# Kernel tuning notes

Hardware: AMD Instinct MI355X
Metric: run time of the kernel (lower is better)

The kernel has to match this reference:

```python
import jax, jax.numpy as jnp
import numpy as np

N_NODES = 100000
N_EDGES = 3200000
IN_FEATS = 128
HIDDEN = 64
N_CLASSES = 16


def gcn_conv(x, src, dst, W, b, num_nodes):
    """PyG GCNConv (default settings): add self-loops, symmetric norm,
    linear transform, scatter-sum aggregation at dst, then bias."""
    # degree counts include self-loops (fill value 1.0)
    deg = jnp.zeros((num_nodes,), x.dtype).at[dst].add(1.0) + 1.0
    dinv = jax.lax.rsqrt(deg)  # deg >= 1, no inf handling needed
    h = x @ W  # [N, out]
    # edge messages: norm(src,dst) * h[src], aggregated at dst
    norm = dinv[src] * dinv[dst]  # [E]
    msg = h[src] * norm[:, None]  # [E, out]
    out = jax.ops.segment_sum(msg, dst, num_segments=num_nodes)
    # self-loop contribution: norm = dinv[i]^2
    out = out + h * (dinv * dinv)[:, None]
    return out + b


def setup_inputs() -> dict:
    key = jax.random.key(0)
    k1, k2, k3, k4 = jax.random.split(key, 4)
    x = jax.random.normal(k1, (N_NODES, IN_FEATS), dtype=jnp.float32)
    edge_index = jax.random.randint(k2, (2, N_EDGES), 0, N_NODES, dtype=jnp.int64)
    W1 = jax.random.normal(k3, (IN_FEATS, HIDDEN), dtype=jnp.float32) * (1.0 / np.sqrt(IN_FEATS))
    b1 = jnp.zeros((HIDDEN,), jnp.float32)
    W2 = jax.random.normal(k4, (HIDDEN, N_CLASSES), dtype=jnp.float32) * (1.0 / np.sqrt(HIDDEN))
    b2 = jnp.zeros((N_CLASSES,), jnp.float32)
    return {"x": x, "edge_index": edge_index, "W1": W1, "b1": b1, "W2": W2, "b2": b2}


def reference(x, edge_index, W1, b1, W2, b2):
    src, dst = edge_index[0], edge_index[1]
    h = gcn_conv(x, src, dst, W1, b1, N_NODES)
    h = jax.nn.relu(h)  # dropout is identity in eval mode
    out = gcn_conv(h, src, dst, W2, b2, N_NODES)
    return out
```

## Files before the change

kernel.cpp:

```cpp
#include <hip/hip_runtime.h>
#include <hip/hip_fp16.h>
#include <stdint.h>

#define N_NODES   100000
#define N_HALF    50000
#define N_EDGES   3200000
#define F_IN      128
#define F_HID     64
#define F_OUT     16

typedef _Float16 h2v __attribute__((ext_vector_type(2)));
typedef _Float16 h4v __attribute__((ext_vector_type(4)));

#define BSHIFT    8
#define NBUCK     391
#define NBLK_P    640
#define CHUNK_E   (N_EDGES / NBLK_P)
#define PSTRIDE   9856

#define G1_TM     128
#define G1_BLOCKS ((N_NODES + G1_TM - 1) / G1_TM)
#define XS_LD     132

#define OFF_RS       0
#define OFF_LEN      400000
#define OFF_DINV     800000
#define OFF_GCNT     1200000
#define OFF_CSR      1201616
#define OFF_HS1      8909008
#define OFF_OUT1A    21709008
#define OFF_OUT1B    34509008
#define OFF_HS2      47309008
#define OFF_PAIRS    OFF_OUT1A

__device__ __forceinline__ int edge_src(const void* ei, int is64, int e) {
    return is64 ? (int)((const long long*)ei)[e] : ((const int*)ei)[e];
}
__device__ __forceinline__ int edge_dst(const void* ei, int is64, int e) {
    return is64 ? (int)((const long long*)ei)[N_EDGES + e]
                : ((const int*)ei)[N_EDGES + e];
}

__global__ __launch_bounds__(256) void k_partition(const void* __restrict__ ei,
                                                   int* __restrict__ gcnt,
                                                   unsigned* __restrict__ pairs) {
    __shared__ unsigned long long st[CHUNK_E];
    __shared__ int h[NBUCK];
    __shared__ int cur[NBUCK];
    __shared__ int is64s;
    int t = threadIdx.x;
    if (t == 0) {
        const unsigned* u = (const unsigned*)ei;
        int ok = 1;
        for (int i = 0; i < 64; ++i) {
            unsigned lo = u[2 * i], hi = u[2 * i + 1];
            if (hi != 0u || lo >= 100000u) { ok = 0; break; }
        }
        is64s = ok;
    }
    for (int i = t; i < NBUCK; i += 256) h[i] = 0;
    __syncthreads();
    int is64 = is64s;
    int base = blockIdx.x * CHUNK_E;
    for (int i = t; i < CHUNK_E; i += 256) {
        int s = edge_src(ei, is64, base + i);
        int d = edge_dst(ei, is64, base + i);
        st[i] = ((unsigned long long)(unsigned)s << 32) | (unsigned)d;
        atomicAdd(&h[d >> BSHIFT], 1);
    }
    __syncthreads();
    for (int i = t; i < NBUCK; i += 256) {
        int c = h[i];
        cur[i] = c ? atomicAdd(&gcnt[i], c) : 0;
    }
    __syncthreads();
    for (int i = t; i < CHUNK_E; i += 256) {
        unsigned long long v = st[i];
        unsigned s = (unsigned)(v >> 32);
        unsigned d = (unsigned)v;
        int b = d >> BSHIFT;
        int p = atomicAdd(&cur[b], 1);
        if (p < PSTRIDE)
            pairs[b * PSTRIDE + p] = (s << 8) | (d & 255u);
    }
}

__global__ __launch_bounds__(512) void k_build(const unsigned* __restrict__ pairs,
                                               const int* __restrict__ gcnt,
                                               int* __restrict__ rowstart,
                                               int* __restrict__ lens,
                                               float* __restrict__ dinv,
                                               unsigned short* __restrict__ csr) {
    __shared__ int c0S[256], c1S[256], scanS[256], pos0[256], pos1[256];
    int b = blockIdx.x, t = threadIdx.x;
    if (t < 256) { c0S[t] = 0; c1S[t] = 0; }
    __syncthreads();
    int tot = gcnt[b]; if (tot > PSTRIDE) tot = PSTRIDE;
    int base = b * PSTRIDE;
    for (int i = t; i < tot; i += 512) {
        unsigned pr = pairs[base + i];
        if ((pr >> 8) < (unsigned)N_HALF) atomicAdd(&c0S[pr & 255u], 1);
        else                              atomicAdd(&c1S[pr & 255u], 1);
    }
    __syncthreads();
    int tpad = 0, p0a = 0;
    if (t < 256) {
        p0a = (c0S[t] + 3) & ~3;
        tpad = p0a + ((c1S[t] + 3) & ~3);
        scanS[t] = tpad;
    }
    __syncthreads();
    for (int off = 1; off < 256; off <<= 1) {
        int add = 0;
        if (t < 256 && t >= off) add = scanS[t - off];
        __syncthreads();
        if (t < 256) scanS[t] += add;
        __syncthreads();
    }
    if (t < 256) {
        int rs = base + scanS[t] - tpad;
        pos0[t] = rs;
        pos1[t] = rs + p0a;
        int d = (b << BSHIFT) + t;
        if (d < N_NODES) {
            rowstart[d] = rs;
            lens[d] = c0S[t] | (c1S[t] << 16);
            dinv[d] = rsqrtf((float)(c0S[t] + c1S[t]) + 1.0f);
        }
    }
    __syncthreads();
    for (int i = t; i < tot; i += 512) {
        unsigned pr = pairs[base + i];
        unsigned s = pr >> 8;
        int d = pr & 255u;
        if (s < (unsigned)N_HALF) {
            int p = atomicAdd(&pos0[d], 1);
            csr[p] = (unsigned short)s;
        } else {
            int p = atomicAdd(&pos1[d], 1);
            csr[p] = (unsigned short)(s - N_HALF);
        }
    }
}

__global__ __launch_bounds__(256) void k_gemm1(const float* __restrict__ x,
                                               const float* __restrict__ W1,
                                               const float* __restrict__ dinv,
                                               __half* __restrict__ hs1) {
    __shared__ float xsT[64 * XS_LD];
    __shared__ float ws[64 * 64];
    int t = threadIdx.x;
    int nblock = blockIdx.x * G1_TM;
    int ng = t >> 4, og = t & 15;
    int n0 = ng * 8;
    float acc[8][4] = {};

    int snode = nblock + (t >> 1);
    int koff = (t & 1) * 32;
    int nl = t >> 1;

    for (int chunk = 0; chunk < 2; ++chunk) {
        int kbase = chunk * 64;
        {
            float4 v[8];
            if (snode < N_NODES) {
                const float4* src = (const float4*)(x + (size_t)snode * F_IN + kbase + koff);
#pragma unroll
                for (int c = 0; c < 8; ++c) v[c] = src[c];
            } else {
#pragma unroll
                for (int c = 0; c < 8; ++c) v[c] = make_float4(0.f, 0.f, 0.f, 0.f);
            }
#pragma unroll
            for (int c = 0; c < 8; ++c) {
                int k = koff + c * 4;
                xsT[(k + 0) * XS_LD + nl] = v[c].x;
                xsT[(k + 1) * XS_LD + nl] = v[c].y;
                xsT[(k + 2) * XS_LD + nl] = v[c].z;
                xsT[(k + 3) * XS_LD + nl] = v[c].w;
            }
        }
        {
            const float4* wsrc = (const float4*)(W1 + kbase * F_HID);
            float4* wdst = (float4*)ws;
#pragma unroll
            for (int c = 0; c < 4; ++c) wdst[c * 256 + t] = wsrc[c * 256 + t];
        }
        __syncthreads();

#pragma unroll 4
        for (int k = 0; k < 64; ++k) {
            const float4* xr = (const float4*)(xsT + k * XS_LD + n0);
            float4 a0 = xr[0], a1 = xr[1];
            float4 bv = *(const float4*)(ws + k * 64 + og * 4);
            float a[8] = {a0.x, a0.y, a0.z, a0.w, a1.x, a1.y, a1.z, a1.w};
            float bb[4] = {bv.x, bv.y, bv.z, bv.w};
#pragma unroll
            for (int i = 0; i < 8; ++i)
#pragma unroll
                for (int j = 0; j < 4; ++j)
                    acc[i][j] += a[i] * bb[j];
        }
        __syncthreads();
    }

#pragma unroll
    for (int i = 0; i < 8; ++i) {
        int node = nblock + n0 + i;
        if (node < N_NODES) {
            float dv = dinv[node];
            union { __half2 h[2]; float2 f; } u;
            u.h[0] = __floats2half2_rn(acc[i][0] * dv, acc[i][1] * dv);
            u.h[1] = __floats2half2_rn(acc[i][2] * dv, acc[i][3] * dv);
            *(float2*)(hs1 + ((size_t)(og >> 3) * N_NODES + node) * 32 + (og & 7) * 4) = u.f;
        }
    }
}

__global__ __launch_bounds__(256) void k_agg1(const __half* __restrict__ hs1,
                                              const unsigned short* __restrict__ csr,
                                              const int* __restrict__ rowstart,
                                              const int* __restrict__ lens,
                                              __half* __restrict__ out1a,
                                              __half* __restrict__ out1b) {
    int bid = blockIdx.x;
    int combo = bid & 3;
    int chunk = combo & 1, half = combo >> 1;
    int nb = bid >> 2;
    int w = threadIdx.x >> 6, lane = threadIdx.x & 63;
    int slot = lane >> 3, fp = lane & 7;
    int n = nb * 32 + w * 8 + slot;
    const char* T = (const char*)hs1
                  + (size_t)chunk * ((size_t)N_NODES * 64)
                  + (size_t)half * ((size_t)N_HALF * 64);
    unsigned fo = fp * 8u;
    int rs = rowstart[n];
    int L = lens[n];
    int c0 = L & 0xffff;
    int start = half ? (rs + ((c0 + 3) & ~3)) : rs;
    int c = half ? (L >> 16) : c0;
    h4v a0 = {(_Float16)0.f, (_Float16)0.f, (_Float16)0.f, (_Float16)0.f};
    h4v a1 = a0, a2 = a0, a3 = a0;
    const unsigned long long* Q = (const unsigned long long*)csr;
    int q0 = start >> 2;
    int nq = c >> 2;
#define ROW1(idx) (*(const h4v*)(T + (unsigned)(idx) * 64u + fo))
    int q = 0;
    unsigned long long ea = 0ull, eb = 0ull;
    if (q + 2 <= nq) { ea = Q[q0]; eb = Q[q0 + 1]; }
    while (q + 2 <= nq) {
        unsigned long long ca = ea, cb = eb;
        q += 2;
        if (q + 2 <= nq) { ea = Q[q0 + q]; eb = Q[q0 + q + 1]; }
        h4v t0 = ROW1(ca & 0xffffu);
        h4v t1 = ROW1((ca >> 16) & 0xffffu);
        h4v t2 = ROW1((ca >> 32) & 0xffffu);
        h4v t3 = ROW1(ca >> 48);
        h4v t4 = ROW1(cb & 0xffffu);
        h4v t5 = ROW1((cb >> 16) & 0xffffu);
        h4v t6 = ROW1((cb >> 32) & 0xffffu);
        h4v t7 = ROW1(cb >> 48);
        a0 += t0; a1 += t1; a2 += t2; a3 += t3;
        a0 += t4; a1 += t5; a2 += t6; a3 += t7;
    }
    if (q < nq) {
        unsigned long long e = Q[q0 + q];
        a0 += ROW1(e & 0xffffu);
        a1 += ROW1((e >> 16) & 0xffffu);
        a2 += ROW1((e >> 32) & 0xffffu);
        a3 += ROW1(e >> 48);
    }
    for (int j = start + (nq << 2); j < start + c; ++j)
        a0 += ROW1(csr[j]);
    if ((n >= N_HALF) == (half != 0))
        a1 += ROW1(n - half * N_HALF);
#undef ROW1
    float s0 = ((float)a0[0] + (float)a1[0]) + ((float)a2[0] + (float)a3[0]);
    float s1 = ((float)a0[1] + (float)a1[1]) + ((float)a2[1] + (float)a3[1]);
    float s2 = ((float)a0[2] + (float)a1[2]) + ((float)a2[2] + (float)a3[2]);
    float s3 = ((float)a0[3] + (float)a1[3]) + ((float)a2[3] + (float)a3[3]);
    union { __half2 h[2]; float2 f; } u;
    u.h[0] = __floats2half2_rn(s0, s1);
    u.h[1] = __floats2half2_rn(s2, s3);
    __half* dst = (half ? out1b : out1a) + (size_t)n * F_HID + chunk * 32 + fp * 4;
    *(float2*)dst = u.f;
}

__global__ __launch_bounds__(256) void k_gemm2(const __half* __restrict__ out1a,
                                               const __half* __restrict__ out1b,
                                               const float* __restrict__ W2,
                                               const float* __restrict__ dinv,
                                               const float* __restrict__ b1,
                                               __half* __restrict__ hs2) {
    __shared__ float ws[F_HID * F_OUT];
    __shared__ float b1s[F_HID];
    int t = threadIdx.x;
    ((float4*)ws)[t] = ((const float4*)W2)[t];
    if (t < 16) ((float4*)b1s)[t] = ((const float4*)b1)[t];
    __syncthreads();
    int tid = blockIdx.x * 256 + t;
    int n = tid >> 2;
    if (n >= N_NODES) return;
    int cq = (tid & 3) << 2;
    float dv = dinv[n];
    const h2v* A = (const h2v*)(out1a + (size_t)n * F_HID);
    const h2v* B = (const h2v*)(out1b + (size_t)n * F_HID);
    float4 acc = make_float4(0.f, 0.f, 0.f, 0.f);
#pragma unroll 4
    for (int k4 = 0; k4 < 16; ++k4) {
        h2v pa0 = A[k4 * 2], pa1 = A[k4 * 2 + 1];
        h2v pb0 = B[k4 * 2], pb1 = B[k4 * 2 + 1];
        float h0 = fmaxf(dv * ((float)pa0.x + (float)pb0.x) + b1s[k4 * 4 + 0], 0.f);
        float h1 = fmaxf(dv * ((float)pa0.y + (float)pb0.y) + b1s[k4 * 4 + 1], 0.f);
        float h2 = fmaxf(dv * ((float)pa1.x + (float)pb1.x) + b1s[k4 * 4 + 2], 0.f);
        float h3 = fmaxf(dv * ((float)pa1.y + (float)pb1.y) + b1s[k4 * 4 + 3], 0.f);
        float4 w0 = *(const float4*)(ws + (k4 * 4 + 0) * F_OUT + cq);
        float4 w1 = *(const float4*)(ws + (k4 * 4 + 1) * F_OUT + cq);
        float4 w2 = *(const float4*)(ws + (k4 * 4 + 2) * F_OUT + cq);
        float4 w3 = *(const float4*)(ws + (k4 * 4 + 3) * F_OUT + cq);
        acc.x += h0 * w0.x + h1 * w1.x + h2 * w2.x + h3 * w3.x;
        acc.y += h0 * w0.y + h1 * w1.y + h2 * w2.y + h3 * w3.y;
        acc.z += h0 * w0.z + h1 * w1.z + h2 * w2.z + h3 * w3.z;
        acc.w += h0 * w0.w + h1 * w1.w + h2 * w2.w + h3 * w3.w;
    }
    union { __half2 h2x[2]; float2 f; } u;
    u.h2x[0] = __floats2half2_rn(acc.x * dv, acc.y * dv);
    u.h2x[1] = __floats2half2_rn(acc.z * dv, acc.w * dv);
    *(float2*)(hs2 + (size_t)n * F_OUT + cq) = u.f;
}

__global__ __launch_bounds__(128) void k_agg2(const __half* __restrict__ hs2,
                                              const unsigned short* __restrict__ csr,
                                              const int* __restrict__ rowstart,
                                              const int* __restrict__ lens,
                                              const float* __restrict__ dinv,
                                              const float* __restrict__ b2,
                                              float* __restrict__ out) {
    int w = threadIdx.x >> 6, lane = threadIdx.x & 63;
    int slot = lane >> 2, fp = lane & 3;
    int n = blockIdx.x * 32 + w * 16 + slot;
    unsigned fo = fp * 8u;
    int rs = rowstart[n];
    int L = lens[n];
    int c0 = L & 0xffff, c1 = L >> 16;
    const unsigned long long* Q = (const unsigned long long*)csr;
    h4v a0 = {(_Float16)0.f, (_Float16)0.f, (_Float16)0.f, (_Float16)0.f};
    h4v a1 = a0, a2 = a0, a3 = a0;
#pragma unroll
    for (int half = 0; half < 2; ++half) {
        const char* T = (const char*)hs2 + (size_t)half * ((size_t)N_HALF * 32);
        int start = half ? (rs + ((c0 + 3) & ~3)) : rs;
        int c = half ? c1 : c0;
        int q0 = start >> 2;
        int nq = c >> 2;
#define ROW2(idx) (*(const h4v*)(T + (unsigned)(idx) * 32u + fo))
        int q = 0;
        unsigned long long ea = 0ull, eb = 0ull;
        if (q + 2 <= nq) { ea = Q[q0]; eb = Q[q0 + 1]; }
        while (q + 2 <= nq) {
            unsigned long long ca = ea, cb = eb;
            q += 2;
            if (q + 2 <= nq) { ea = Q[q0 + q]; eb = Q[q0 + q + 1]; }
            h4v t0 = ROW2(ca & 0xffffu);
            h4v t1 = ROW2((ca >> 16) & 0xffffu);
            h4v t2 = ROW2((ca >> 32) & 0xffffu);
            h4v t3 = ROW2(ca >> 48);
            h4v t4 = ROW2(cb & 0xffffu);
            h4v t5 = ROW2((cb >> 16) & 0xffffu);
            h4v t6 = ROW2((cb >> 32) & 0xffffu);
            h4v t7 = ROW2(cb >> 48);
            a0 += t0; a1 += t1; a2 += t2; a3 += t3;
            a0 += t4; a1 += t5; a2 += t6; a3 += t7;
        }
        if (q < nq) {
            unsigned long long e = Q[q0 + q];
            a0 += ROW2(e & 0xffffu);
            a1 += ROW2((e >> 16) & 0xffffu);
            a2 += ROW2((e >> 32) & 0xffffu);
            a3 += ROW2(e >> 48);
        }
        for (int j = start + (nq << 2); j < start + c; ++j)
            a0 += ROW2(csr[j]);
#undef ROW2
    }
    a1 += *(const h4v*)((const char*)hs2 + (unsigned)n * 32u + fo);
    float dv = dinv[n];
    int fb = fp * 4;
    float s0 = ((float)a0[0] + (float)a1[0]) + ((float)a2[0] + (float)a3[0]);
    float s1 = ((float)a0[1] + (float)a1[1]) + ((float)a2[1] + (float)a3[1]);
    float s2 = ((float)a0[2] + (float)a1[2]) + ((float)a2[2] + (float)a3[2]);
    float s3 = ((float)a0[3] + (float)a1[3]) + ((float)a2[3] + (float)a3[3]);
    float4 bv = *(const float4*)(b2 + fb);
    float4 o = make_float4(dv * s0 + bv.x, dv * s1 + bv.y,
                           dv * s2 + bv.z, dv * s3 + bv.w);
    *(float4*)(out + (size_t)n * F_OUT + fb) = o;
}

extern "C" void kernel_launch(void* const* d_in, const int* in_sizes, int n_in,
                              void* d_out, int out_size, void* d_ws, size_t ws_size,
                              hipStream_t stream) {
    const float* x  = (const float*)d_in[0];
    const void*  ei = d_in[1];
    const float* W1 = (const float*)d_in[2];
    const float* b1 = (const float*)d_in[3];
    const float* W2 = (const float*)d_in[4];
    const float* b2 = (const float*)d_in[5];
    float* out = (float*)d_out;

    char* ws = (char*)d_ws;
    int*            rowstart = (int*)(ws + OFF_RS);
    int*            lens     = (int*)(ws + OFF_LEN);
    float*          dinv     = (float*)(ws + OFF_DINV);
    int*            gcnt     = (int*)(ws + OFF_GCNT);
    unsigned short* csr      = (unsigned short*)(ws + OFF_CSR);
    __half*         hs1      = (__half*)(ws + OFF_HS1);
    __half*         out1a    = (__half*)(ws + OFF_OUT1A);
    __half*         out1b    = (__half*)(ws + OFF_OUT1B);
    __half*         hs2      = (__half*)(ws + OFF_HS2);
    unsigned*       pairs    = (unsigned*)(ws + OFF_PAIRS);

    hipMemsetAsync(gcnt, 0, NBUCK * sizeof(int), stream);
    k_partition<<<NBLK_P, 256, 0, stream>>>(ei, gcnt, pairs);
    k_build    <<<NBUCK, 512, 0, stream>>>(pairs, gcnt, rowstart, lens, dinv, csr);

    k_gemm1<<<G1_BLOCKS, 256, 0, stream>>>(x, W1, dinv, hs1);
    k_agg1 <<<12500, 256, 0, stream>>>(hs1, csr, rowstart, lens, out1a, out1b);
    k_gemm2<<<(N_NODES * 4 + 255) / 256, 256, 0, stream>>>(out1a, out1b, W2, dinv, b1, hs2);
    k_agg2 <<<3125, 128, 0, stream>>>(hs2, csr, rowstart, lens, dinv, b2, out);
}
```

Measured before the change: 288.7 us.

## Partition CSR by source into quarters and gather full 64-wide rows in aggregation

The CSR is now split into four source-node quarters instead of two halves, and hs1 switches from two 32-feature chunks to a row-major 64-feature layout. Layer-1 aggregation runs as two launches, each covering two quarters, and reads whole 128-byte rows with 8-wide half vectors. The second launch adds its partial sums to the first launch's fp16 output. The aim is a smaller gather working set per pass (25k rows, about 3.2MB) so it stays cache-resident, without re-reading the CSR per feature chunk. Nontemporal loads and stores are added for streaming indices and outputs. The cost is an extra read-modify-write of the intermediates and an extra fp16 rounding step.

```diff
diff --git a/kernel.cpp b/kernel.cpp
--- a/kernel.cpp
+++ b/kernel.cpp
@@ -3,7 +3,7 @@
 #include <stdint.h>
 
 #define N_NODES   100000
-#define N_HALF    50000
+#define N_QUAR    25000
 #define N_EDGES   3200000
 #define F_IN      128
 #define F_HID     64
@@ -11,26 +11,29 @@
 
 typedef _Float16 h2v __attribute__((ext_vector_type(2)));
 typedef _Float16 h4v __attribute__((ext_vector_type(4)));
+typedef _Float16 h8v __attribute__((ext_vector_type(8)));
+typedef float    f4v __attribute__((ext_vector_type(4)));
 
 #define BSHIFT    8
 #define NBUCK     391
 #define NBLK_P    640
 #define CHUNK_E   (N_EDGES / NBLK_P)
-#define PSTRIDE   9856
+#define PSTRIDE   10752
 
 #define G1_TM     128
 #define G1_BLOCKS ((N_NODES + G1_TM - 1) / G1_TM)
 #define XS_LD     132
 
 #define OFF_RS       0
-#define OFF_LEN      400000
-#define OFF_DINV     800000
-#define OFF_GCNT     1200000
-#define OFF_CSR      1201616
-#define OFF_HS1      8909008
-#define OFF_OUT1A    21709008
-#define OFF_OUT1B    34509008
-#define OFF_HS2      47309008
+#define OFF_LENA     400000
+#define OFF_LENB     800000
+#define OFF_DINV     1200000
+#define OFF_GCNT     1600000
+#define OFF_CSR      1601616
+#define OFF_HS1      10009680
+#define OFF_OUT1A    22809680
+#define OFF_OUT1B    35609680
+#define OFF_HS2      OFF_HS1
 #define OFF_PAIRS    OFF_OUT1A
 
 __device__ __forceinline__ int edge_src(const void* ei, int is64, int e) {
@@ -88,25 +91,30 @@
 __global__ __launch_bounds__(512) void k_build(const unsigned* __restrict__ pairs,
                                                const int* __restrict__ gcnt,
                                                int* __restrict__ rowstart,
-                                               int* __restrict__ lens,
+                                               int* __restrict__ lensA,
+                                               int* __restrict__ lensB,
                                                float* __restrict__ dinv,
                                                unsigned short* __restrict__ csr) {
-    __shared__ int c0S[256], c1S[256], scanS[256], pos0[256], pos1[256];
+    __shared__ int cQ[4][256];
+    __shared__ int posQ[4][256];
+    __shared__ int scanS[256];
     int b = blockIdx.x, t = threadIdx.x;
-    if (t < 256) { c0S[t] = 0; c1S[t] = 0; }
+    if (t < 256) { cQ[0][t] = 0; cQ[1][t] = 0; cQ[2][t] = 0; cQ[3][t] = 0; }
     __syncthreads();
     int tot = gcnt[b]; if (tot > PSTRIDE) tot = PSTRIDE;
     int base = b * PSTRIDE;
     for (int i = t; i < tot; i += 512) {
         unsigned pr = pairs[base + i];
-        if ((pr >> 8) < (unsigned)N_HALF) atomicAdd(&c0S[pr & 255u], 1);
-        else                              atomicAdd(&c1S[pr & 255u], 1);
-    }
-    __syncthreads();
-    int tpad = 0, p0a = 0;
+        unsigned s = pr >> 8;
+        int q = (s >= 25000u) + (s >= 50000u) + (s >= 75000u);
+        atomicAdd(&cQ[q][pr & 255u], 1);
+    }
+    __syncthreads();
+    int tpad = 0, p0 = 0, p1 = 0, p2 = 0;
     if (t < 256) {
-        p0a = (c0S[t] + 3) & ~3;
-        tpad = p0a + ((c1S[t] + 3) & ~3);
+        int c0 = cQ[0][t], c1 = cQ[1][t], c2 = cQ[2][t], c3 = cQ[3][t];
+        p0 = (c0 + 3) & ~3; p1 = (c1 + 3) & ~3; p2 = (c2 + 3) & ~3;
+        tpad = p0 + p1 + p2 + ((c3 + 3) & ~3);
         scanS[t] = tpad;
     }
     __syncthreads();
@@ -119,13 +127,17 @@
     }
     if (t < 256) {
         int rs = base + scanS[t] - tpad;
-        pos0[t] = rs;
-        pos1[t] = rs + p0a;
+        posQ[0][t] = rs;
+        posQ[1][t] = rs + p0;
+        posQ[2][t] = rs + p0 + p1;
+        posQ[3][t] = rs + p0 + p1 + p2;
         int d = (b << BSHIFT) + t;
         if (d < N_NODES) {
+            int c0 = cQ[0][t], c1 = cQ[1][t], c2 = cQ[2][t], c3 = cQ[3][t];
             rowstart[d] = rs;
-            lens[d] = c0S[t] | (c1S[t] << 16);
-            dinv[d] = rsqrtf((float)(c0S[t] + c1S[t]) + 1.0f);
+            lensA[d] = c0 | (c1 << 16);
+            lensB[d] = c2 | (c3 << 16);
+            dinv[d] = rsqrtf((float)(c0 + c1 + c2 + c3) + 1.0f);
         }
     }
     __syncthreads();
@@ -133,13 +145,9 @@
         unsigned pr = pairs[base + i];
         unsigned s = pr >> 8;
         int d = pr & 255u;
-        if (s < (unsigned)N_HALF) {
-            int p = atomicAdd(&pos0[d], 1);
-            csr[p] = (unsigned short)s;
-        } else {
-            int p = atomicAdd(&pos1[d], 1);
-            csr[p] = (unsigned short)(s - N_HALF);
-        }
+        int q = (s >= 25000u) + (s >= 50000u) + (s >= 75000u);
+        int p = atomicAdd(&posQ[q][d], 1);
+        csr[p] = (unsigned short)(s - (unsigned)q * 25000u);
     }
 }
 
@@ -212,7 +220,7 @@
             union { __half2 h[2]; float2 f; } u;
             u.h[0] = __floats2half2_rn(acc[i][0] * dv, acc[i][1] * dv);
             u.h[1] = __floats2half2_rn(acc[i][2] * dv, acc[i][3] * dv);
-            *(float2*)(hs1 + ((size_t)(og >> 3) * N_NODES + node) * 32 + (og & 7) * 4) = u.f;
+            *(float2*)(hs1 + (size_t)node * 64 + og * 4) = u.f;
         }
     }
 }
@@ -220,70 +228,87 @@
 __global__ __launch_bounds__(256) void k_agg1(const __half* __restrict__ hs1,
                                               const unsigned short* __restrict__ csr,
                                               const int* __restrict__ rowstart,
-                                              const int* __restrict__ lens,
+                                              const int* __restrict__ lensA,
+                                              const int* __restrict__ lensB,
                                               __half* __restrict__ out1a,
-                                              __half* __restrict__ out1b) {
+                                              __half* __restrict__ out1b,
+                                              int qbase, int addold) {
     int bid = blockIdx.x;
-    int combo = bid & 3;
-    int chunk = combo & 1, half = combo >> 1;
-    int nb = bid >> 2;
+    int combo = bid & 1;
+    int q = qbase + combo;
+    int nb = bid >> 1;
     int w = threadIdx.x >> 6, lane = threadIdx.x & 63;
     int slot = lane >> 3, fp = lane & 7;
     int n = nb * 32 + w * 8 + slot;
-    const char* T = (const char*)hs1
-                  + (size_t)chunk * ((size_t)N_NODES * 64)
-                  + (size_t)half * ((size_t)N_HALF * 64);
-    unsigned fo = fp * 8u;
-    int rs = rowstart[n];
-    int L = lens[n];
-    int c0 = L & 0xffff;
-    int start = half ? (rs + ((c0 + 3) & ~3)) : rs;
-    int c = half ? (L >> 16) : c0;
-    h4v a0 = {(_Float16)0.f, (_Float16)0.f, (_Float16)0.f, (_Float16)0.f};
-    h4v a1 = a0, a2 = a0, a3 = a0;
+    const char* Tb = (const char*)hs1 + (size_t)q * (N_QUAR * 128);
+    unsigned fo = fp * 16u;
+    int rs = __builtin_nontemporal_load(rowstart + n);
+    int LA = __builtin_nontemporal_load(lensA + n);
+    int LB = __builtin_nontemporal_load(lensB + n);
+    int c0 = LA & 0xffff, c1 = (LA >> 16) & 0xffff;
+    int c2 = LB & 0xffff, c3 = LB >> 16;
+    int start = rs, c = c0;
+    if (q >= 1) { start += (c0 + 3) & ~3; c = c1; }
+    if (q >= 2) { start += (c1 + 3) & ~3; c = c2; }
+    if (q >= 3) { start += (c2 + 3) & ~3; c = c3; }
+    h8v a0 = {(_Float16)0.f, (_Float16)0.f, (_Float16)0.f, (_Float16)0.f,
+              (_Float16)0.f, (_Float16)0.f, (_Float16)0.f, (_Float16)0.f};
+    h8v a1 = a0, a2 = a0, a3 = a0;
     const unsigned long long* Q = (const unsigned long long*)csr;
-    int q0 = start >> 2;
+    int q0w = start >> 2;
     int nq = c >> 2;
-#define ROW1(idx) (*(const h4v*)(T + (unsigned)(idx) * 64u + fo))
-    int q = 0;
+#define ROW1(idx) (*(const h8v*)(Tb + (unsigned)(idx) * 128u + fo))
+    int i = 0;
     unsigned long long ea = 0ull, eb = 0ull;
-    if (q + 2 <= nq) { ea = Q[q0]; eb = Q[q0 + 1]; }
-    while (q + 2 <= nq) {
+    if (i + 2 <= nq) {
+        ea = __builtin_nontemporal_load(Q + q0w);
+        eb = __builtin_nontemporal_load(Q + q0w + 1);
+    }
+    while (i + 2 <= nq) {
         unsigned long long ca = ea, cb = eb;
-        q += 2;
-        if (q + 2 <= nq) { ea = Q[q0 + q]; eb = Q[q0 + q + 1]; }
-        h4v t0 = ROW1(ca & 0xffffu);
-        h4v t1 = ROW1((ca >> 16) & 0xffffu);
-        h4v t2 = ROW1((ca >> 32) & 0xffffu);
-        h4v t3 = ROW1(ca >> 48);
-        h4v t4 = ROW1(cb & 0xffffu);
-        h4v t5 = ROW1((cb >> 16) & 0xffffu);
-        h4v t6 = ROW1((cb >> 32) & 0xffffu);
-        h4v t7 = ROW1(cb >> 48);
+        i += 2;
+        if (i + 2 <= nq) {
+            ea = __builtin_nontemporal_load(Q + q0w + i);
+            eb = __builtin_nontemporal_load(Q + q0w + i + 1);
+        }
+        h8v t0 = ROW1(ca & 0xffffu);
+        h8v t1 = ROW1((ca >> 16) & 0xffffu);
+        h8v t2 = ROW1((ca >> 32) & 0xffffu);
+        h8v t3 = ROW1(ca >> 48);
+        h8v t4 = ROW1(cb & 0xffffu);
+        h8v t5 = ROW1((cb >> 16) & 0xffffu);
+        h8v t6 = ROW1((cb >> 32) & 0xffffu);
+        h8v t7 = ROW1(cb >> 48);
         a0 += t0; a1 += t1; a2 += t2; a3 += t3;
         a0 += t4; a1 += t5; a2 += t6; a3 += t7;
     }
-    if (q < nq) {
-        unsigned long long e = Q[q0 + q];
+    if (i < nq) {
+        unsigned long long e = __builtin_nontemporal_load(Q + q0w + i);
         a0 += ROW1(e & 0xffffu);
         a1 += ROW1((e >> 16) & 0xffffu);
         a2 += ROW1((e >> 32) & 0xffffu);
         a3 += ROW1(e >> 48);
     }
     for (int j = start + (nq << 2); j < start + c; ++j)
-        a0 += ROW1(csr[j]);
-    if ((n >= N_HALF) == (half != 0))
-        a1 += ROW1(n - half * N_HALF);
+        a0 += ROW1(__builtin_nontemporal_load(csr + j));
+    int nl = n - q * N_QUAR;
+    if ((unsigned)nl < (unsigned)N_QUAR)
+        a1 += ROW1(nl);
 #undef ROW1
-    float s0 = ((float)a0[0] + (float)a1[0]) + ((float)a2[0] + (float)a3[0]);
-    float s1 = ((float)a0[1] + (float)a1[1]) + ((float)a2[1] + (float)a3[1]);
-    float s2 = ((float)a0[2] + (float)a1[2]) + ((float)a2[2] + (float)a3[2]);
-    float s3 = ((float)a0[3] + (float)a1[3]) + ((float)a2[3] + (float)a3[3]);
-    union { __half2 h[2]; float2 f; } u;
-    u.h[0] = __floats2half2_rn(s0, s1);
-    u.h[1] = __floats2half2_rn(s2, s3);
-    __half* dst = (half ? out1b : out1a) + (size_t)n * F_HID + chunk * 32 + fp * 4;
-    *(float2*)dst = u.f;
+    float s[8];
+#pragma unroll
+    for (int k = 0; k < 8; ++k)
+        s[k] = ((float)a0[k] + (float)a1[k]) + ((float)a2[k] + (float)a3[k]);
+    __half* dst = (combo ? out1b : out1a) + (size_t)n * F_HID + fp * 8;
+    if (addold) {
+        h8v old = *(const h8v*)dst;
+#pragma unroll
+        for (int k = 0; k < 8; ++k) s[k] += (float)old[k];
+    }
+    h8v o;
+#pragma unroll
+    for (int k = 0; k < 8; ++k) o[k] = (_Float16)s[k];
+    *(h8v*)dst = o;
 }
 
 __global__ __launch_bounds__(256) void k_gemm2(const __half* __restrict__ out1a,
@@ -332,7 +357,8 @@
 __global__ __launch_bounds__(128) void k_agg2(const __half* __restrict__ hs2,
                                               const unsigned short* __restrict__ csr,
                                               const int* __restrict__ rowstart,
-                                              const int* __restrict__ lens,
+                                              const int* __restrict__ lensA,
+                                              const int* __restrict__ lensB,
                                               const float* __restrict__ dinv,
                                               const float* __restrict__ b2,
                                               float* __restrict__ out) {
@@ -340,27 +366,36 @@
     int slot = lane >> 2, fp = lane & 3;
     int n = blockIdx.x * 32 + w * 16 + slot;
     unsigned fo = fp * 8u;
-    int rs = rowstart[n];
-    int L = lens[n];
-    int c0 = L & 0xffff, c1 = L >> 16;
+    int rs = __builtin_nontemporal_load(rowstart + n);
+    int LA = __builtin_nontemporal_load(lensA + n);
+    int LB = __builtin_nontemporal_load(lensB + n);
+    int cs[4];
+    cs[0] = LA & 0xffff; cs[1] = (LA >> 16) & 0xffff;
+    cs[2] = LB & 0xffff; cs[3] = LB >> 16;
     const unsigned long long* Q = (const unsigned long long*)csr;
     h4v a0 = {(_Float16)0.f, (_Float16)0.f, (_Float16)0.f, (_Float16)0.f};
     h4v a1 = a0, a2 = a0, a3 = a0;
-#pragma unroll
-    for (int half = 0; half < 2; ++half) {
-        const char* T = (const char*)hs2 + (size_t)half * ((size_t)N_HALF * 32);
-        int start = half ? (rs + ((c0 + 3) & ~3)) : rs;
-        int c = half ? c1 : c0;
+    int start = rs;
+#pragma unroll
+    for (int qq = 0; qq < 4; ++qq) {
+        const char* T = (const char*)hs2 + (size_t)qq * (N_QUAR * 32);
+        int c = cs[qq];
         int q0 = start >> 2;
         int nq = c >> 2;
 #define ROW2(idx) (*(const h4v*)(T + (unsigned)(idx) * 32u + fo))
-        int q = 0;
+        int i = 0;
         unsigned long long ea = 0ull, eb = 0ull;
-        if (q + 2 <= nq) { ea = Q[q0]; eb = Q[q0 + 1]; }
-        while (q + 2 <= nq) {
+        if (i + 2 <= nq) {
+            ea = __builtin_nontemporal_load(Q + q0);
+            eb = __builtin_nontemporal_load(Q + q0 + 1);
+        }
+        while (i + 2 <= nq) {
             unsigned long long ca = ea, cb = eb;
-            q += 2;
-            if (q + 2 <= nq) { ea = Q[q0 + q]; eb = Q[q0 + q + 1]; }
+            i += 2;
+            if (i + 2 <= nq) {
+                ea = __builtin_nontemporal_load(Q + q0 + i);
+                eb = __builtin_nontemporal_load(Q + q0 + i + 1);
+            }
             h4v t0 = ROW2(ca & 0xffffu);
             h4v t1 = ROW2((ca >> 16) & 0xffffu);
             h4v t2 = ROW2((ca >> 32) & 0xffffu);
@@ -372,16 +407,17 @@
             a0 += t0; a1 += t1; a2 += t2; a3 += t3;
             a0 += t4; a1 += t5; a2 += t6; a3 += t7;
         }
-        if (q < nq) {
-            unsigned long long e = Q[q0 + q];
+        if (i < nq) {
+            unsigned long long e = __builtin_nontemporal_load(Q + q0 + i);
             a0 += ROW2(e & 0xffffu);
             a1 += ROW2((e >> 16) & 0xffffu);
             a2 += ROW2((e >> 32) & 0xffffu);
             a3 += ROW2(e >> 48);
         }
         for (int j = start + (nq << 2); j < start + c; ++j)
-            a0 += ROW2(csr[j]);
+            a0 += ROW2(__builtin_nontemporal_load(csr + j));
 #undef ROW2
+        start += (c + 3) & ~3;
     }
     a1 += *(const h4v*)((const char*)hs2 + (unsigned)n * 32u + fo);
     float dv = dinv[n];
@@ -391,9 +427,12 @@
     float s2 = ((float)a0[2] + (float)a1[2]) + ((float)a2[2] + (float)a3[2]);
     float s3 = ((float)a0[3] + (float)a1[3]) + ((float)a2[3] + (float)a3[3]);
     float4 bv = *(const float4*)(b2 + fb);
-    float4 o = make_float4(dv * s0 + bv.x, dv * s1 + bv.y,
-                           dv * s2 + bv.z, dv * s3 + bv.w);
-    *(float4*)(out + (size_t)n * F_OUT + fb) = o;
+    f4v o;
+    o[0] = dv * s0 + bv.x;
+    o[1] = dv * s1 + bv.y;
+    o[2] = dv * s2 + bv.z;
+    o[3] = dv * s3 + bv.w;
+    __builtin_nontemporal_store(o, (f4v*)(out + (size_t)n * F_OUT + fb));
 }
 
 extern "C" void kernel_launch(void* const* d_in, const int* in_sizes, int n_in,
@@ -409,7 +448,8 @@
 
     char* ws = (char*)d_ws;
     int*            rowstart = (int*)(ws + OFF_RS);
-    int*            lens     = (int*)(ws + OFF_LEN);
+    int*            lensA    = (int*)(ws + OFF_LENA);
+    int*            lensB    = (int*)(ws + OFF_LENB);
     float*          dinv     = (float*)(ws + OFF_DINV);
     int*            gcnt     = (int*)(ws + OFF_GCNT);
     unsigned short* csr      = (unsigned short*)(ws + OFF_CSR);
@@ -419,12 +459,13 @@
     __half*         hs2      = (__half*)(ws + OFF_HS2);
     unsigned*       pairs    = (unsigned*)(ws + OFF_PAIRS);
 
-    hipMemsetAsync(gcnt, 0, NBUCK * sizeof(int), stream);
+    (void)hipMemsetAsync(gcnt, 0, NBUCK * sizeof(int), stream);
     k_partition<<<NBLK_P, 256, 0, stream>>>(ei, gcnt, pairs);
-    k_build    <<<NBUCK, 512, 0, stream>>>(pairs, gcnt, rowstart, lens, dinv, csr);
+    k_build    <<<NBUCK, 512, 0, stream>>>(pairs, gcnt, rowstart, lensA, lensB, dinv, csr);
 
     k_gemm1<<<G1_BLOCKS, 256, 0, stream>>>(x, W1, dinv, hs1);
-    k_agg1 <<<12500, 256, 0, stream>>>(hs1, csr, rowstart, lens, out1a, out1b);
+    k_agg1 <<<6250, 256, 0, stream>>>(hs1, csr, rowstart, lensA, lensB, out1a, out1b, 0, 0);
+    k_agg1 <<<6250, 256, 0, stream>>>(hs1, csr, rowstart, lensA, lensB, out1a, out1b, 2, 1);
     k_gemm2<<<(N_NODES * 4 + 255) / 256, 256, 0, stream>>>(out1a, out1b, W2, dinv, b1, hs2);
-    k_agg2 <<<3125, 128, 0, stream>>>(hs2, csr, rowstart, lens, dinv, b2, out);
-}
+    k_agg2 <<<3125, 128, 0, stream>>>(hs2, csr, rowstart, lensA, lensB, dinv, b2, out);
+}
```

Result: slower. 324.0 us (+12.2%).
